# Performance work log

Hardware: AMD Instinct MI355X
Metric: run time of the kernel (lower is better)

## Reference

```python
import jax, jax.numpy as jnp
import numpy as np

B, N, D, H, DEG = 2, 20000, 256, 8, 8
E = N * DEG
EPS = 1e-3  # keras LayerNormalization default epsilon


def layer_norm(x, gamma, beta):
    mu = jnp.mean(x, axis=-1, keepdims=True)
    var = jnp.mean(jnp.square(x - mu), axis=-1, keepdims=True)
    return (x - mu) * jax.lax.rsqrt(var + EPS) * gamma + beta


def setup_inputs() -> dict:
    key = jax.random.key(0)
    ks = jax.random.split(key, 8)
    x = jax.random.normal(ks[0], (B, N, D), dtype=jnp.float32)
    # edge list sorted by source node; every node has DEG out-edges so
    # segment_sum covers all N segments (matches tf.math.segment_sum semantics)
    src = jnp.repeat(jnp.arange(N, dtype=jnp.int64), DEG)
    dst = jax.random.randint(ks[1], (E,), 0, N, dtype=jnp.int64)
    edges = jnp.stack([src, dst], axis=1)  # [E, 2]
    scale = 0.05
    wq = jax.random.normal(ks[2], (D, D), dtype=jnp.float32) * scale
    wk = jax.random.normal(ks[3], (D, D), dtype=jnp.float32) * scale
    wv = jax.random.normal(ks[4], (D, D), dtype=jnp.float32) * scale
    wo = jax.random.normal(ks[5], (D, D), dtype=jnp.float32) * scale
    zeros = jnp.zeros((D,), dtype=jnp.float32)
    ones = jnp.ones((D,), dtype=jnp.float32)
    return {
        "x": x, "edges": edges,
        "wq": wq, "bq": zeros, "wk": wk, "bk": zeros,
        "wv": wv, "bv": zeros, "wo": wo, "bo": zeros,
        "gamma1": ones, "beta1": zeros, "gamma2": ones, "beta2": zeros,
    }


def reference(x, edges, wq, bq, wk, bk, wv, bv, wo, bo, gamma1, beta1, gamma2, beta2):
    b, n, d = x.shape
    h, dh = H, D // H
    xn = layer_norm(x, gamma1, beta1)                      # [B,N,D]
    # QKV projections, split heads, move node axis to front: [N,B,H,dh]
    def proj(w, bias):
        y = (xn @ w + bias).reshape(b, n, h, dh)
        return jnp.transpose(y, (1, 0, 2, 3))
    q, k, v = proj(wq, bq), proj(wk, bk), proj(wv, bv)
    src, dst = edges[:, 0], edges[:, 1]
    q_part = q[src]                                         # [E,B,H,dh]
    k_part = k[dst]
    v_part = v[dst]
    logits = jnp.sum(q_part * k_part, axis=-1, keepdims=True) / jnp.sqrt(
        jnp.asarray(dh, dtype=x.dtype))                     # [E,B,H,1]
    w = jnp.exp(logits)                                     # unnormalized softmax (as in source)
    num = jax.ops.segment_sum(v_part * w, src, num_segments=n)  # [N,B,H,dh]
    den = jax.ops.segment_sum(w, src, num_segments=n)           # [N,B,H,1]
    attn = num / den
    attn = jnp.transpose(attn, (1, 0, 2, 3)).reshape(b, n, d)   # [B,N,D]
    concat = xn + attn                                      # residual uses normed input (source reassigns `inputs`)
    out = layer_norm(concat, gamma2, beta2)
    out = jax.nn.relu(out @ wo + bo)
    return out + concat
```

## Files before the change

### kernel.cpp

```cpp
#include <hip/hip_runtime.h>


typedef __bf16 bf16x8 __attribute__((ext_vector_type(8)));
typedef float  f32x4  __attribute__((ext_vector_type(4)));

__device__ __forceinline__ float bf2f(unsigned short u) {
    union { unsigned int i; float f; } v; v.i = ((unsigned int)u) << 16; return v.f;
}
__device__ __forceinline__ unsigned short f2bf(float f) {
    union { float f; unsigned int i; } v; v.f = f;
    unsigned int x = v.i;
    unsigned int r = (x + 0x7FFFu + ((x >> 16) & 1u)) >> 16;
    return (unsigned short)r;
}

#define NNODE 20000
#define ROWS  40000
#define DMODEL 256

__global__ __launch_bounds__(256) void prep_ln1_kernel(
    const float* __restrict__ wq, const float* __restrict__ wk,
    const float* __restrict__ wv, const float* __restrict__ wo,
    const float* __restrict__ bq, const float* __restrict__ bk,
    const float* __restrict__ bv, const float* __restrict__ bo,
    const float* __restrict__ x,
    const float* __restrict__ g1, const float* __restrict__ b1,
    unsigned short* __restrict__ Wqkvt,
    unsigned short* __restrict__ Wot,
    float* __restrict__ biasq,
    float* __restrict__ biaso,
    unsigned short* __restrict__ xn)
{
    if (blockIdx.x < 1024) {
        int idx = blockIdx.x * 256 + threadIdx.x;
        if (idx < 768 * 256) {
            int n = idx >> 8, k = idx & 255;
            int sel = n >> 8, nl = n & 255;
            const float* w = (sel == 0) ? wq : (sel == 1) ? wk : wv;
            Wqkvt[idx] = f2bf(w[k * 256 + nl]);
        } else {
            int idx2 = idx - 768 * 256;
            int n = idx2 >> 8, k = idx2 & 255;
            Wot[idx2] = f2bf(wo[k * 256 + n]);
        }
        if (idx < 768) {
            const float* bb = (idx < 256) ? bq : (idx < 512) ? bk : bv;
            biasq[idx] = bb[idx & 255];
        }
        if (idx >= 768 && idx < 1024) biaso[idx - 768] = bo[idx - 768];
        return;
    }
    int wave = threadIdx.x >> 6, lane = threadIdx.x & 63;
    int sub = lane >> 5, hl = lane & 31;
    int m = (blockIdx.x - 1024) * 8 + wave * 2 + sub;
    const float* xp = x + (size_t)m * DMODEL + hl * 8;
    float4 x0 = *(const float4*)xp;
    float4 x1 = *(const float4*)(xp + 4);
    float f[8] = {x0.x, x0.y, x0.z, x0.w, x1.x, x1.y, x1.z, x1.w};
    float s = 0.f, ss = 0.f;
    #pragma unroll
    for (int t = 0; t < 8; ++t) { s += f[t]; ss += f[t]*f[t]; }
    #pragma unroll
    for (int mk = 1; mk < 32; mk <<= 1) { s += __shfl_xor(s, mk); ss += __shfl_xor(ss, mk); }
    float mu  = s * (1.f/256.f);
    float var = ss * (1.f/256.f) - mu*mu;
    float rs  = rsqrtf(var + 1e-3f);
    float4 g0 = *(const float4*)(g1 + hl * 8);
    float4 g1v = *(const float4*)(g1 + hl * 8 + 4);
    float4 b0 = *(const float4*)(b1 + hl * 8);
    float4 b1v = *(const float4*)(b1 + hl * 8 + 4);
    float gg[8] = {g0.x, g0.y, g0.z, g0.w, g1v.x, g1v.y, g1v.z, g1v.w};
    float bb[8] = {b0.x, b0.y, b0.z, b0.w, b1v.x, b1v.y, b1v.z, b1v.w};
    unsigned short o[8];
    #pragma unroll
    for (int t = 0; t < 8; ++t) o[t] = f2bf((f[t] - mu) * rs * gg[t] + bb[t]);
    *(int4*)(xn + (size_t)m * DMODEL + hl * 8) = *(const int4*)o;
}

#define LDS_W 72
#define MFMA_BF16(d, a, b) d = __builtin_amdgcn_mfma_f32_16x16x32_bf16(a, b, d, 0, 0, 0)

template<bool EPI>
__global__ __launch_bounds__(512, 2) void gemm_kernel(
    const unsigned short* __restrict__ A,
    const unsigned short* __restrict__ Bt,
    const float* __restrict__ bias,
    void* __restrict__ C,
    const unsigned short* __restrict__ resid,
    int M, int Ncols)
{
    __shared__ unsigned short As[128 * LDS_W];
    __shared__ unsigned short Bs[128 * LDS_W];
    int tid  = threadIdx.x;
    int wave = tid >> 6, lane = tid & 63;
    int quad = lane >> 4, l16 = lane & 15;

    int nt_total = Ncols >> 7;
    int nwg = gridDim.x;
    int xcd = blockIdx.x & 7, loc = blockIdx.x >> 3;
    int qq = nwg >> 3, rr = nwg & 7;
    int wid = (xcd < rr) ? (xcd * (qq + 1) + loc)
                         : (rr * (qq + 1) + (xcd - rr) * qq + loc);
    int mt = wid / nt_total;
    int nt = wid - mt * nt_total;
    int m0 = mt * 128, n0 = nt * 128;
    int wm = (wave >> 1) * 32, wn = (wave & 1) * 64;

    int srow = tid >> 2;
    int scol = (tid & 3) * 16;
    int arow = m0 + srow; if (arow >= M) arow = M - 1;
    const unsigned short* ArowP = A  + (size_t)arow * 256 + scol;
    const unsigned short* BrowP = Bt + (size_t)(n0 + srow) * 256 + scol;
    unsigned short* AsP = &As[srow * LDS_W + scol];
    unsigned short* BsP = &Bs[srow * LDS_W + scol];

    f32x4 acc00 = {}, acc01 = {}, acc02 = {}, acc03 = {};
    f32x4 acc10 = {}, acc11 = {}, acc12 = {}, acc13 = {};

    int4 va0 = *(const int4*)(ArowP);
    int4 va1 = *(const int4*)(ArowP + 8);
    int4 vb0 = *(const int4*)(BrowP);
    int4 vb1 = *(const int4*)(BrowP + 8);

    for (int kt = 0; kt < 4; ++kt) {
        __syncthreads();
        *(int4*)(AsP)     = va0;
        *(int4*)(AsP + 8) = va1;
        *(int4*)(BsP)     = vb0;
        *(int4*)(BsP + 8) = vb1;
        __syncthreads();
        if (kt < 3) {
            const unsigned short* ap = ArowP + (kt + 1) * 64;
            const unsigned short* bp = BrowP + (kt + 1) * 64;
            va0 = *(const int4*)(ap);
            va1 = *(const int4*)(ap + 8);
            vb0 = *(const int4*)(bp);
            vb1 = *(const int4*)(bp + 8);
        }
        #pragma unroll
        for (int ks = 0; ks < 64; ks += 32) {
            bf16x8 a0 = *(const bf16x8*)&As[(wm +  0 + l16) * LDS_W + ks + quad * 8];
            bf16x8 a1 = *(const bf16x8*)&As[(wm + 16 + l16) * LDS_W + ks + quad * 8];
            bf16x8 b0 = *(const bf16x8*)&Bs[(wn +  0 + l16) * LDS_W + ks + quad * 8];
            bf16x8 b1 = *(const bf16x8*)&Bs[(wn + 16 + l16) * LDS_W + ks + quad * 8];
            bf16x8 b2 = *(const bf16x8*)&Bs[(wn + 32 + l16) * LDS_W + ks + quad * 8];
            bf16x8 b3 = *(const bf16x8*)&Bs[(wn + 48 + l16) * LDS_W + ks + quad * 8];
            MFMA_BF16(acc00, a0, b0); MFMA_BF16(acc01, a0, b1);
            MFMA_BF16(acc02, a0, b2); MFMA_BF16(acc03, a0, b3);
            MFMA_BF16(acc10, a1, b0); MFMA_BF16(acc11, a1, b1);
            MFMA_BF16(acc12, a1, b2); MFMA_BF16(acc13, a1, b3);
        }
    }

#define EPI_STORE(accv, R, CC) do {                                          \
        int col = n0 + wn + (CC) * 16 + l16;                                 \
        float bb = bias[col];                                                \
        int rowb = m0 + wm + (R) * 16 + quad * 4;                            \
        _Pragma("unroll")                                                    \
        for (int rr = 0; rr < 4; ++rr) {                                     \
            int row = rowb + rr;                                             \
            if (row < M) {                                                   \
                float v = (accv)[rr] + bb;                                   \
                if (EPI) {                                                   \
                    v = fmaxf(v, 0.f);                                       \
                    v += bf2f(resid[(size_t)row * 256 + col]);               \
                    ((float*)C)[(size_t)row * Ncols + col] = v;              \
                } else {                                                     \
                    ((unsigned short*)C)[(size_t)row * Ncols + col] = f2bf(v);\
                }                                                            \
            }                                                                \
        }                                                                    \
    } while (0)

    EPI_STORE(acc00, 0, 0); EPI_STORE(acc01, 0, 1); EPI_STORE(acc02, 0, 2); EPI_STORE(acc03, 0, 3);
    EPI_STORE(acc10, 1, 0); EPI_STORE(acc11, 1, 1); EPI_STORE(acc12, 1, 2); EPI_STORE(acc13, 1, 3);
#undef EPI_STORE
}

__global__ __launch_bounds__(1024) void attn_kernel(
    const unsigned short* __restrict__ qkv,
    const int* __restrict__ edges,
    const unsigned short* __restrict__ xn,
    const float* __restrict__ g2, const float* __restrict__ b2,
    unsigned short* __restrict__ concat,
    unsigned short* __restrict__ h2,
    int node0)
{
    int wave = threadIdx.x >> 6, lane = threadIdx.x & 63;
    int i = node0 + blockIdx.x * 16 + wave;
    int b = lane >> 5, hl = lane & 31;
    size_t m = (size_t)b * NNODE + i;

    int jv = 0;
    if (lane < 8) jv = edges[2 * (i * 8 + lane) + 1];

    int4 qi = *(const int4*)(qkv + m * 768 + hl * 8);
    int4 xi = *(const int4*)(xn + m * DMODEL + hl * 8);
    const unsigned short* qs = (const unsigned short*)&qi;
    float qf[8];
    #pragma unroll
    for (int t = 0; t < 8; ++t) qf[t] = bf2f(qs[t]);

#define KVLOAD(E)                                                                  \
    int j##E = __shfl(jv, E);                                                      \
    const unsigned short* kp##E = qkv + ((size_t)b * NNODE + j##E) * 768 + 256 + hl * 8; \
    int4 KI##E = *(const int4*)(kp##E);                                            \
    int4 VI##E = *(const int4*)(kp##E + 256);
    KVLOAD(0) KVLOAD(1) KVLOAD(2) KVLOAD(3)
    KVLOAD(4) KVLOAD(5) KVLOAD(6) KVLOAD(7)
#undef KVLOAD

    float acc[8] = {};
    float den = 0.f;
    const float scale = 0.17677669529663687f;
#define EDGE(E) do {                                                         \
        const unsigned short* ks = (const unsigned short*)&KI##E;            \
        const unsigned short* vs = (const unsigned short*)&VI##E;            \
        float dot = 0.f;                                                     \
        _Pragma("unroll")                                                    \
        for (int t = 0; t < 8; ++t) dot += qf[t] * bf2f(ks[t]);              \
        dot += __shfl_xor(dot, 1);                                           \
        dot += __shfl_xor(dot, 2);               \
        float w = __expf(dot * scale);                                       \
        _Pragma("unroll")                                                    \
        for (int t = 0; t < 8; ++t) acc[t] += w * bf2f(vs[t]);               \
        den += w;                                                            \
    } while (0)
    EDGE(0); EDGE(1); EDGE(2); EDGE(3);
    EDGE(4); EDGE(5); EDGE(6); EDGE(7);
#undef EDGE
    float inv = 1.f / den;

    const unsigned short* xs = (const unsigned short*)&xi;
    float c[8], s = 0.f, ss = 0.f;
    #pragma unroll
    for (int t = 0; t < 8; ++t) { c[t] = bf2f(xs[t]) + acc[t] * inv; s += c[t]; ss += c[t]*c[t]; }
    #pragma unroll
    for (int mk = 1; mk < 32; mk <<= 1) { s += __shfl_xor(s, mk); ss += __shfl_xor(ss, mk); }
    float mu  = s * (1.f/256.f);
    float var = ss * (1.f/256.f) - mu*mu;
    float rs  = rsqrtf(var + 1e-3f);

    float4 ga = *(const float4*)(g2 + hl * 8);
    float4 gb = *(const float4*)(g2 + hl * 8 + 4);
    float4 ba = *(const float4*)(b2 + hl * 8);
    float4 bb = *(const float4*)(b2 + hl * 8 + 4);
    float gg[8] = {ga.x, ga.y, ga.z, ga.w, gb.x, gb.y, gb.z, gb.w};
    float bv[8] = {ba.x, ba.y, ba.z, ba.w, bb.x, bb.y, bb.z, bb.w};
    unsigned short oc[8], oh[8];
    #pragma unroll
    for (int t = 0; t < 8; ++t) {
        oc[t] = f2bf(c[t]);
        oh[t] = f2bf((c[t] - mu) * rs * gg[t] + bv[t]);
    }
    *(int4*)(concat + m * DMODEL + hl * 8) = *(const int4*)oc;
    *(int4*)(h2     + m * DMODEL + hl * 8) = *(const int4*)oh;
}

extern "C" void kernel_launch(void* const* d_in, const int* in_sizes, int n_in,
                              void* d_out, int out_size, void* d_ws, size_t ws_size,
                              hipStream_t stream)
{
    const float* x   = (const float*)d_in[0];
    const int* edges = (const int*)d_in[1];
    const float* wq = (const float*)d_in[2];
    const float* bq = (const float*)d_in[3];
    const float* wk = (const float*)d_in[4];
    const float* bk = (const float*)d_in[5];
    const float* wv = (const float*)d_in[6];
    const float* bv = (const float*)d_in[7];
    const float* wo = (const float*)d_in[8];
    const float* bo = (const float*)d_in[9];
    const float* g1 = (const float*)d_in[10];
    const float* b1 = (const float*)d_in[11];
    const float* g2 = (const float*)d_in[12];
    const float* b2 = (const float*)d_in[13];

    char* ws = (char*)d_ws;
    unsigned short* Wqkvt = (unsigned short*)(ws);
    unsigned short* Wot   = (unsigned short*)(ws + 393216);
    float* biasq          = (float*)(ws + 393216 + 131072);
    float* biaso          = (float*)(ws + 393216 + 131072 + 3072);
    size_t off = 393216 + 131072 + 4096;
    unsigned short* xn     = (unsigned short*)(ws + off); off += (size_t)ROWS * DMODEL * 2;
    unsigned short* qkv    = (unsigned short*)(ws + off); off += (size_t)ROWS * 768 * 2;
    unsigned short* concat = (unsigned short*)(ws + off); off += (size_t)ROWS * DMODEL * 2;
    unsigned short* h2     = (unsigned short*)(ws + off); off += (size_t)ROWS * DMODEL * 2;

    prep_ln1_kernel<<<1024 + ROWS / 8, 256, 0, stream>>>(
        wq, wk, wv, wo, bq, bk, bv, bo, x, g1, b1, Wqkvt, Wot, biasq, biaso, xn);
    gemm_kernel<false><<<dim3(313 * 6), 512, 0, stream>>>(xn, Wqkvt, biasq, qkv, nullptr, ROWS, 768);
    attn_kernel<<<625, 1024, 0, stream>>>(qkv, edges, xn, g2, b2, concat, h2, 0);
    attn_kernel<<<625, 1024, 0, stream>>>(qkv, edges, xn, g2, b2, concat, h2, 10000);
    gemm_kernel<true><<<dim3(313 * 2), 512, 0, stream>>>(h2, Wot, biaso, d_out, concat, ROWS, 256);
}
```

Baseline: 230.7 us.

## Load full K=256 tiles into LDS once and merge attention launches

The GEMM kernel now stages the whole 128x256 A and B tiles into shared memory in a single pass with one barrier, then runs all eight MFMA k-steps without further synchronization, replacing the four-stage register-prefetched loop. This raises LDS use to about 135 KB per block, so launch bounds drop to one block per CU, trading occupancy and load/compute overlap for fewer barriers. The two half-node attention launches are also merged into a single launch over all nodes to cut launch overhead and tail effects.

```diff
diff --git a/kernel.cpp b/kernel.cpp
--- a/kernel.cpp
+++ b/kernel.cpp
@@ -77,11 +77,11 @@
     *(int4*)(xn + (size_t)m * DMODEL + hl * 8) = *(const int4*)o;
 }
 
-#define LDS_W 72
+#define LDSW 264
 #define MFMA_BF16(d, a, b) d = __builtin_amdgcn_mfma_f32_16x16x32_bf16(a, b, d, 0, 0, 0)
 
 template<bool EPI>
-__global__ __launch_bounds__(512, 2) void gemm_kernel(
+__global__ __launch_bounds__(512, 1) void gemm_kernel(
     const unsigned short* __restrict__ A,
     const unsigned short* __restrict__ Bt,
     const float* __restrict__ bias,
@@ -89,8 +89,8 @@
     const unsigned short* __restrict__ resid,
     int M, int Ncols)
 {
-    __shared__ unsigned short As[128 * LDS_W];
-    __shared__ unsigned short Bs[128 * LDS_W];
+    __shared__ unsigned short As[128 * LDSW];
+    __shared__ unsigned short Bs[128 * LDSW];
     int tid  = threadIdx.x;
     int wave = tid >> 6, lane = tid & 63;
     int quad = lane >> 4, l16 = lane & 15;
@@ -107,49 +107,41 @@
     int wm = (wave >> 1) * 32, wn = (wave & 1) * 64;
 
     int srow = tid >> 2;
-    int scol = (tid & 3) * 16;
+    int c16  = (tid & 3) * 16;
     int arow = m0 + srow; if (arow >= M) arow = M - 1;
-    const unsigned short* ArowP = A  + (size_t)arow * 256 + scol;
-    const unsigned short* BrowP = Bt + (size_t)(n0 + srow) * 256 + scol;
-    unsigned short* AsP = &As[srow * LDS_W + scol];
-    unsigned short* BsP = &Bs[srow * LDS_W + scol];
+    const unsigned short* Ap = A  + (size_t)arow * 256 + c16;
+    const unsigned short* Bp = Bt + (size_t)(n0 + srow) * 256 + c16;
+    unsigned short* AsP = &As[srow * LDSW + c16];
+    unsigned short* BsP = &Bs[srow * LDSW + c16];
+    #pragma unroll
+    for (int j = 0; j < 4; ++j) {
+        int4 a0 = *(const int4*)(Ap + j * 64);
+        int4 a1 = *(const int4*)(Ap + j * 64 + 8);
+        int4 b0 = *(const int4*)(Bp + j * 64);
+        int4 b1 = *(const int4*)(Bp + j * 64 + 8);
+        *(int4*)(AsP + j * 64)     = a0;
+        *(int4*)(AsP + j * 64 + 8) = a1;
+        *(int4*)(BsP + j * 64)     = b0;
+        *(int4*)(BsP + j * 64 + 8) = b1;
+    }
+    __syncthreads();
 
     f32x4 acc00 = {}, acc01 = {}, acc02 = {}, acc03 = {};
     f32x4 acc10 = {}, acc11 = {}, acc12 = {}, acc13 = {};
 
-    int4 va0 = *(const int4*)(ArowP);
-    int4 va1 = *(const int4*)(ArowP + 8);
-    int4 vb0 = *(const int4*)(BrowP);
-    int4 vb1 = *(const int4*)(BrowP + 8);
-
-    for (int kt = 0; kt < 4; ++kt) {
-        __syncthreads();
-        *(int4*)(AsP)     = va0;
-        *(int4*)(AsP + 8) = va1;
-        *(int4*)(BsP)     = vb0;
-        *(int4*)(BsP + 8) = vb1;
-        __syncthreads();
-        if (kt < 3) {
-            const unsigned short* ap = ArowP + (kt + 1) * 64;
-            const unsigned short* bp = BrowP + (kt + 1) * 64;
-            va0 = *(const int4*)(ap);
-            va1 = *(const int4*)(ap + 8);
-            vb0 = *(const int4*)(bp);
-            vb1 = *(const int4*)(bp + 8);
-        }
-        #pragma unroll
-        for (int ks = 0; ks < 64; ks += 32) {
-            bf16x8 a0 = *(const bf16x8*)&As[(wm +  0 + l16) * LDS_W + ks + quad * 8];
-            bf16x8 a1 = *(const bf16x8*)&As[(wm + 16 + l16) * LDS_W + ks + quad * 8];
-            bf16x8 b0 = *(const bf16x8*)&Bs[(wn +  0 + l16) * LDS_W + ks + quad * 8];
-            bf16x8 b1 = *(const bf16x8*)&Bs[(wn + 16 + l16) * LDS_W + ks + quad * 8];
-            bf16x8 b2 = *(const bf16x8*)&Bs[(wn + 32 + l16) * LDS_W + ks + quad * 8];
-            bf16x8 b3 = *(const bf16x8*)&Bs[(wn + 48 + l16) * LDS_W + ks + quad * 8];
-            MFMA_BF16(acc00, a0, b0); MFMA_BF16(acc01, a0, b1);
-            MFMA_BF16(acc02, a0, b2); MFMA_BF16(acc03, a0, b3);
-            MFMA_BF16(acc10, a1, b0); MFMA_BF16(acc11, a1, b1);
-            MFMA_BF16(acc12, a1, b2); MFMA_BF16(acc13, a1, b3);
-        }
+    #pragma unroll
+    for (int ks = 0; ks < 256; ks += 32) {
+        int ca = ks + quad * 8;
+        bf16x8 a0 = *(const bf16x8*)&As[(wm +  0 + l16) * LDSW + ca];
+        bf16x8 a1 = *(const bf16x8*)&As[(wm + 16 + l16) * LDSW + ca];
+        bf16x8 b0 = *(const bf16x8*)&Bs[(wn +  0 + l16) * LDSW + ca];
+        bf16x8 b1 = *(const bf16x8*)&Bs[(wn + 16 + l16) * LDSW + ca];
+        bf16x8 b2 = *(const bf16x8*)&Bs[(wn + 32 + l16) * LDSW + ca];
+        bf16x8 b3 = *(const bf16x8*)&Bs[(wn + 48 + l16) * LDSW + ca];
+        MFMA_BF16(acc00, a0, b0); MFMA_BF16(acc01, a0, b1);
+        MFMA_BF16(acc02, a0, b2); MFMA_BF16(acc03, a0, b3);
+        MFMA_BF16(acc10, a1, b0); MFMA_BF16(acc11, a1, b1);
+        MFMA_BF16(acc12, a1, b2); MFMA_BF16(acc13, a1, b3);
     }
 
 #define EPI_STORE(accv, R, CC) do {                                          \
@@ -183,11 +175,10 @@
     const unsigned short* __restrict__ xn,
     const float* __restrict__ g2, const float* __restrict__ b2,
     unsigned short* __restrict__ concat,
-    unsigned short* __restrict__ h2,
-    int node0)
+    unsigned short* __restrict__ h2)
 {
     int wave = threadIdx.x >> 6, lane = threadIdx.x & 63;
-    int i = node0 + blockIdx.x * 16 + wave;
+    int i = blockIdx.x * 16 + wave;
     int b = lane >> 5, hl = lane & 31;
     size_t m = (size_t)b * NNODE + i;
 
@@ -290,7 +281,6 @@
     prep_ln1_kernel<<<1024 + ROWS / 8, 256, 0, stream>>>(
         wq, wk, wv, wo, bq, bk, bv, bo, x, g1, b1, Wqkvt, Wot, biasq, biaso, xn);
     gemm_kernel<false><<<dim3(313 * 6), 512, 0, stream>>>(xn, Wqkvt, biasq, qkv, nullptr, ROWS, 768);
-    attn_kernel<<<625, 1024, 0, stream>>>(qkv, edges, xn, g2, b2, concat, h2, 0);
-    attn_kernel<<<625, 1024, 0, stream>>>(qkv, edges, xn, g2, b2, concat, h2, 10000);
+    attn_kernel<<<NNODE / 16, 1024, 0, stream>>>(qkv, edges, xn, g2, b2, concat, h2);
     gemm_kernel<true><<<dim3(313 * 2), 512, 0, stream>>>(h2, Wot, biaso, d_out, concat, ROWS, 256);
 }
```

New measurement: 247.8 us. 7.4% more time.
